# Kernel optimization log

Measured on AMD Instinct MI355X. Metric: run time of the kernel, lower is better.

Reference implementation:

```python
import jax, jax.numpy as jnp
import numpy as np
from jax.scipy.linalg import solve_triangular

H, VD, M = 16, 64, 128
RIDGE = 0.01


def setup_inputs() -> dict:
    key = jax.random.key(0)
    ks = jax.random.split(key, 9)
    B, L, HD = 4, 2048, 1024
    s = 1.0 / np.sqrt(HD).astype(np.float32)
    return {
        "x": jax.random.normal(ks[0], (B, L, HD), dtype=jnp.float32),
        "cur_k": jnp.zeros((1,), dtype=jnp.float32),
        "input_mask": jnp.ones((B, L), dtype=jnp.float32),
        "Wq": jax.random.normal(ks[1], (HD, HD), dtype=jnp.float32) * s,
        "Wk": jax.random.normal(ks[2], (HD, HD), dtype=jnp.float32) * s,
        "Wv": jax.random.normal(ks[3], (HD, HD), dtype=jnp.float32) * s,
        "Wo": jax.random.normal(ks[4], (HD, HD), dtype=jnp.float32) * s,
        "bo": jax.random.normal(ks[5], (HD,), dtype=jnp.float32) * s,
        "rff_W": jax.random.normal(ks[6], (H, VD, M), dtype=jnp.float32),  # / lengthscale=1.0
        "rff_b": 2.0 * np.pi * jax.random.uniform(ks[7], (H, M), dtype=jnp.float32),
    }


def reference(x, cur_k, input_mask, Wq, Wk, Wv, Wo, bo, rff_W, rff_b):
    B, L, HD = x.shape
    scale = jnp.asarray(1.0 / np.sqrt(M), dtype=x.dtype)
    M2 = 2 * M

    def heads(t):  # [B,L,HD] -> [B,H,L,VD]
        return t.reshape(B, L, H, VD).transpose(0, 2, 1, 3)

    q = heads(x @ Wq.T)
    k = heads(x @ Wk.T)
    v = heads(x @ Wv.T)

    mask = input_mask[:, :L].astype(x.dtype)
    qmask = mask[:, None, :, None]  # [B,1,L,1]

    def rff(X):  # [B,H,L,VD] -> [B,H,L,2M]
        proj = jnp.einsum('bhld,hdm->bhlm', X, rff_W) + rff_b[None, :, None, :]
        return scale * jnp.concatenate([jnp.cos(proj), jnp.sin(proj)], axis=-1)

    PhiQ = rff(q)
    PhiK_w = rff(k) * qmask
    V_w = v * qmask

    G = jnp.einsum('bhlm,bhln->bhmn', PhiK_w, PhiK_w)  # [B,H,2M,2M]
    G = G + RIDGE * jnp.eye(M2, dtype=x.dtype)
    T = jnp.einsum('bhlm,bhld->bhmd', PhiK_w, V_w)      # [B,H,2M,VD]

    Lch = jnp.linalg.cholesky(G)
    y = solve_triangular(Lch, T, lower=True)
    W = solve_triangular(jnp.swapaxes(Lch, -2, -1), y, lower=False)

    out = jnp.einsum('bhlm,bhmd->bhld', PhiQ, W)        # [B,H,L,VD]
    # unsqueeze sample dim, permute to [B,1,L,H,VD], flatten heads -> [B,1,L,HD]
    samples = jnp.transpose(out, (0, 2, 1, 3)).reshape(B, L, HD)[:, None]
    samples = samples @ Wo.T + bo                        # W_O (dropout: eval no-op)
    samples = samples * qmask                            # [B,1,L,1] broadcast
    return samples
```

## Files before the change

### kernel.cpp

```cpp
#include <hip/hip_runtime.h>
#include <math.h>

#define B_ 4
#define L_ 2048
#define HD_ 1024
#define H_ 16
#define VD_ 64
#define M_ 128
#define M2_ 256
#define RIDGE_ 0.01f
#define SCALE_ 0.08838834764831845f

typedef unsigned short u16;
typedef __attribute__((ext_vector_type(8))) short short8;
typedef __attribute__((ext_vector_type(4))) float floatx4;

__device__ __forceinline__ u16 f2bf(float x) {
  unsigned u = __float_as_uint(x);
  unsigned r = u + 0x7fff + ((u >> 16) & 1);
  return (u16)(r >> 16);
}
__device__ __forceinline__ float bf2f(u16 h) {
  return __uint_as_float(((unsigned)h) << 16);
}
__device__ __forceinline__ void gload_lds16(const u16* g, u16* l) {
  __builtin_amdgcn_global_load_lds(
      (const __attribute__((address_space(1))) unsigned int*)g,
      (__attribute__((address_space(3))) unsigned int*)l, 16, 0, 0);
}
__device__ __forceinline__ void split4(float4 f, ushort4* h, float4* r) {
  h->x = f2bf(f.x); h->y = f2bf(f.y); h->z = f2bf(f.z); h->w = f2bf(f.w);
  r->x = f.x - bf2f(h->x); r->y = f.y - bf2f(h->y);
  r->z = f.z - bf2f(h->z); r->w = f.w - bf2f(h->w);
}
#define WAITVM(N) asm volatile("s_waitcnt vmcnt(" #N ")" ::: "memory")
__device__ __forceinline__ void barf() {
  asm volatile("" ::: "memory");
  __builtin_amdgcn_s_barrier();
  asm volatile("" ::: "memory");
}
__device__ __forceinline__ void swz2d(int* bx, int* by) {
  int gx = gridDim.x;
  int nwg = gx * gridDim.y;
  int orig = (*by) * gx + (*bx);
  int wg = (orig & 7) * (nwg >> 3) + (orig >> 3);
  *bx = wg % gx;
  *by = wg / gx;
}

__global__ __launch_bounds__(256) void cvt_split_kernel(
    const float* __restrict__ src, u16* __restrict__ hi, u16* __restrict__ lo, int n4)
{
  int i = blockIdx.x * 256 + threadIdx.x;
  if (i < n4) {
    float4 f = ((const float4*)src)[i];
    ushort4 hv; float4 r;
    split4(f, &hv, &r);
    ushort4 lv = {f2bf(r.x), f2bf(r.y), f2bf(r.z), f2bf(r.w)};
    ((ushort4*)hi)[i] = hv;
    ((ushort4*)lo)[i] = lv;
  }
}

__global__ __launch_bounds__(256) void mfma_nt(
    const u16* __restrict__ A0, const u16* __restrict__ B0,
    float* __restrict__ C, int Ndim, int Kdim, int ldA, int ldB,
    const float* __restrict__ bias, const float* __restrict__ mask)
{
  __shared__ __align__(16) u16 a_sm[2][4096];
  __shared__ __align__(16) u16 b_sm[2][4096];
  const int tid = threadIdx.x;
  const int wave = tid >> 6, lane = tid & 63;
  int bx = blockIdx.x, by = blockIdx.y;
  swz2d(&bx, &by);
  const int m0 = by * 128, n0 = bx * 128;
  const int wrow = (wave >> 1) * 64, wcol = (wave & 1) * 64;
  const int fm = lane & 15, q = lane >> 4;
  const int lofs = wave * 1024;

  floatx4 acc[4][4];
#pragma unroll
  for (int i = 0; i < 4; ++i)
#pragma unroll
    for (int j = 0; j < 4; ++j) acc[i][j] = (floatx4){0.f, 0.f, 0.f, 0.f};

  const u16* Ag0 = A0 + (long)(m0 + lane) * ldA + wave * 8;
  const u16* Ag1 = A0 + (long)(m0 + 64 + lane) * ldA + wave * 8;
  const u16* Bg0 = B0 + (long)(n0 + lane) * ldB + wave * 8;
  const u16* Bg1 = B0 + (long)(n0 + 64 + lane) * ldB + wave * 8;

  auto stage = [&](int d, int k0) {
    gload_lds16(Ag0 + k0, &a_sm[d][lofs]);
    gload_lds16(Ag1 + k0, &a_sm[d][lofs + 512]);
    gload_lds16(Bg0 + k0, &b_sm[d][lofs]);
    gload_lds16(Bg1 + k0, &b_sm[d][lofs + 512]);
  };
  auto compute = [&](int d) {
    short8 af[4], bfv[4];
#pragma unroll
    for (int i = 0; i < 4; ++i)
      af[i] = *(const short8*)&a_sm[d][(q * 128 + wrow + i * 16 + fm) * 8];
#pragma unroll
    for (int j = 0; j < 4; ++j)
      bfv[j] = *(const short8*)&b_sm[d][(q * 128 + wcol + j * 16 + fm) * 8];
    __builtin_amdgcn_s_setprio(1);
#pragma unroll
    for (int i = 0; i < 4; ++i)
#pragma unroll
      for (int j = 0; j < 4; ++j)
        acc[i][j] = __builtin_amdgcn_mfma_f32_16x16x32_bf16(af[i], bfv[j], acc[i][j], 0, 0, 0);
    __builtin_amdgcn_s_setprio(0);
  };

  stage(0, 0);
  stage(1, 32);
  for (int k = 0; k + 64 < Kdim; k += 64) {
    WAITVM(4); barf();
    compute(0);
    barf();
    stage(0, k + 64);
    WAITVM(4); barf();
    compute(1);
    barf();
    stage(1, k + 96);
  }
  WAITVM(4); barf();
  compute(0);
  barf();
  WAITVM(0); barf();
  compute(1);

  const int colb = n0 + wcol + fm;
  const int rbase = m0 + wrow + (lane >> 4) * 4;
#pragma unroll
  for (int j = 0; j < 4; ++j) {
    int cg = colb + j * 16;
    float bb = bias ? bias[cg] : 0.f;
#pragma unroll
    for (int i = 0; i < 4; ++i) {
#pragma unroll
      for (int r = 0; r < 4; ++r) {
        int row = rbase + i * 16 + r;
        float val = acc[i][j][r];
        if (bias) val = (val + bb) * mask[row];
        C[(long)row * Ndim + cg] = val;
      }
    }
  }
}

__global__ __launch_bounds__(256) void mfma_qk3(
    const u16* __restrict__ Ah, const u16* __restrict__ Al,
    const u16* __restrict__ Bh, const u16* __restrict__ Bl,
    float* __restrict__ Cq, float* __restrict__ Ck)
{
  __shared__ __align__(16) u16 ah_sm[2][4096], al_sm[2][4096];
  __shared__ __align__(16) u16 bh_sm[2][4096], bl_sm[2][4096];
  const int tid = threadIdx.x;
  const int wave = tid >> 6, lane = tid & 63;
  int bx = blockIdx.x, by = blockIdx.y;
  swz2d(&bx, &by);
  const int m0 = by * 128, n0 = bx * 128;
  const int wrow = (wave >> 1) * 64, wcol = (wave & 1) * 64;
  const int fm = lane & 15, q = lane >> 4;
  const int lofs = wave * 1024;

  floatx4 acc[4][4];
#pragma unroll
  for (int i = 0; i < 4; ++i)
#pragma unroll
    for (int j = 0; j < 4; ++j) acc[i][j] = (floatx4){0.f, 0.f, 0.f, 0.f};

  const long a0o = (long)(m0 + lane) * 1024 + wave * 8;
  const long a1o = (long)(m0 + 64 + lane) * 1024 + wave * 8;
  const long b0o = (long)(n0 + lane) * 1024 + wave * 8;
  const long b1o = (long)(n0 + 64 + lane) * 1024 + wave * 8;

  auto stage = [&](int d, int k0) {
    gload_lds16(Ah + a0o + k0, &ah_sm[d][lofs]);
    gload_lds16(Ah + a1o + k0, &ah_sm[d][lofs + 512]);
    gload_lds16(Al + a0o + k0, &al_sm[d][lofs]);
    gload_lds16(Al + a1o + k0, &al_sm[d][lofs + 512]);
    gload_lds16(Bh + b0o + k0, &bh_sm[d][lofs]);
    gload_lds16(Bh + b1o + k0, &bh_sm[d][lofs + 512]);
    gload_lds16(Bl + b0o + k0, &bl_sm[d][lofs]);
    gload_lds16(Bl + b1o + k0, &bl_sm[d][lofs + 512]);
  };
  auto compute = [&](int d) {
    short8 afh[4], afl[4], bfh[4], bfl[4];
#pragma unroll
    for (int i = 0; i < 4; ++i) {
      afh[i] = *(const short8*)&ah_sm[d][(q * 128 + wrow + i * 16 + fm) * 8];
      afl[i] = *(const short8*)&al_sm[d][(q * 128 + wrow + i * 16 + fm) * 8];
    }
#pragma unroll
    for (int j = 0; j < 4; ++j) {
      bfh[j] = *(const short8*)&bh_sm[d][(q * 128 + wcol + j * 16 + fm) * 8];
      bfl[j] = *(const short8*)&bl_sm[d][(q * 128 + wcol + j * 16 + fm) * 8];
    }
    __builtin_amdgcn_s_setprio(1);
#pragma unroll
    for (int i = 0; i < 4; ++i)
#pragma unroll
      for (int j = 0; j < 4; ++j) {
        acc[i][j] = __builtin_amdgcn_mfma_f32_16x16x32_bf16(afh[i], bfh[j], acc[i][j], 0, 0, 0);
        acc[i][j] = __builtin_amdgcn_mfma_f32_16x16x32_bf16(afl[i], bfh[j], acc[i][j], 0, 0, 0);
        acc[i][j] = __builtin_amdgcn_mfma_f32_16x16x32_bf16(afh[i], bfl[j], acc[i][j], 0, 0, 0);
      }
    __builtin_amdgcn_s_setprio(0);
  };

  stage(0, 0);
  stage(1, 32);
  for (int k = 0; k + 64 < 1024; k += 64) {
    WAITVM(8); barf();
    compute(0);
    barf();
    stage(0, k + 64);
    WAITVM(8); barf();
    compute(1);
    barf();
    stage(1, k + 96);
  }
  WAITVM(8); barf();
  compute(0);
  barf();
  WAITVM(0); barf();
  compute(1);

  float* Cp; int cb;
  if (n0 < 1024) { Cp = Cq; cb = n0; }
  else           { Cp = Ck; cb = n0 - 1024; }
  const int colb = cb + wcol + fm;
  const int rbase = m0 + wrow + (lane >> 4) * 4;
#pragma unroll
  for (int j = 0; j < 4; ++j) {
    int cg = colb + j * 16;
#pragma unroll
    for (int i = 0; i < 4; ++i)
#pragma unroll
      for (int r = 0; r < 4; ++r)
        Cp[(long)(rbase + i * 16 + r) * 1024 + cg] = acc[i][j][r];
  }
}

__global__ __launch_bounds__(256) void rff_k_t(
    const float* __restrict__ src, const float* __restrict__ mask,
    const float* __restrict__ rffW, const float* __restrict__ rffb,
    u16* __restrict__ pkh, u16* __restrict__ pkl, int b0)
{
  __shared__ __align__(16) float w_lds[64][132];
  __shared__ __align__(16) float x_lds[64][68];
  __shared__ float b_lds[128];
  const int l0 = blockIdx.x * 64;
  const int h = blockIdx.y, b = b0 + blockIdx.z;
  const int zloc = blockIdx.z * 16 + h;
  const int tid = threadIdx.x;

  const float* wsrc = rffW + h * 8192;
  for (int f = tid * 4; f < 8192; f += 1024) {
    int d = f >> 7, m = f & 127;
    *(float4*)&w_lds[d][m] = *(const float4*)&wsrc[f];
  }
  if (tid < 128) b_lds[tid] = rffb[h * 128 + tid];
  {
    int r = tid >> 2, c0 = (tid & 3) * 16;
    const float* srow = src + (long)(b * L_ + l0 + r) * 1024 + h * VD_ + c0;
    *(float4*)&x_lds[r][c0 + 0]  = *(const float4*)(srow + 0);
    *(float4*)&x_lds[r][c0 + 4]  = *(const float4*)(srow + 4);
    *(float4*)&x_lds[r][c0 + 8]  = *(const float4*)(srow + 8);
    *(float4*)&x_lds[r][c0 + 12] = *(const float4*)(srow + 12);
  }
  __syncthreads();

  const int ty = tid >> 4, tx = tid & 15;
  float acc[4][8];
  {
    float4 bb0 = *(const float4*)&b_lds[4 * tx];
    float4 bb1 = *(const float4*)&b_lds[4 * tx + 64];
#pragma unroll
    for (int i = 0; i < 4; ++i) {
      acc[i][0] = bb0.x; acc[i][1] = bb0.y; acc[i][2] = bb0.z; acc[i][3] = bb0.w;
      acc[i][4] = bb1.x; acc[i][5] = bb1.y; acc[i][6] = bb1.z; acc[i][7] = bb1.w;
    }
  }
#pragma unroll 8
  for (int kk = 0; kk < 64; ++kk) {
    float4 w0 = *(const float4*)&w_lds[kk][4 * tx];
    float4 w1 = *(const float4*)&w_lds[kk][4 * tx + 64];
    float xv[4];
#pragma unroll
    for (int i = 0; i < 4; ++i) xv[i] = x_lds[4 * ty + i][kk];
#pragma unroll
    for (int i = 0; i < 4; ++i) {
      acc[i][0] = fmaf(xv[i], w0.x, acc[i][0]);
      acc[i][1] = fmaf(xv[i], w0.y, acc[i][1]);
      acc[i][2] = fmaf(xv[i], w0.z, acc[i][2]);
      acc[i][3] = fmaf(xv[i], w0.w, acc[i][3]);
      acc[i][4] = fmaf(xv[i], w1.x, acc[i][4]);
      acc[i][5] = fmaf(xv[i], w1.y, acc[i][5]);
      acc[i][6] = fmaf(xv[i], w1.z, acc[i][6]);
      acc[i][7] = fmaf(xv[i], w1.w, acc[i][7]);
    }
  }
  float fi[4];
#pragma unroll
  for (int i = 0; i < 4; ++i) fi[i] = SCALE_ * mask[b * L_ + l0 + 4 * ty + i];
  float cvv[4][8], svv[4][8];
#pragma unroll
  for (int i = 0; i < 4; ++i)
#pragma unroll
    for (int jj = 0; jj < 8; ++jj) {
      float sv, cv;
      sincosf(acc[i][jj], &sv, &cv);
      cvv[i][jj] = cv * fi[i];
      svv[i][jj] = sv * fi[i];
    }
  const long lbase = l0 + 4 * ty;
  const long zbase = (long)zloc * 655360;
#pragma unroll
  for (int jj = 0; jj < 8; ++jj) {
    int mcol = (jj < 4) ? (4 * tx + jj) : (64 + 4 * tx + (jj - 4));
    ushort4 h4, l4;
    h4.x = f2bf(cvv[0][jj]); l4.x = f2bf(cvv[0][jj] - bf2f(h4.x));
    h4.y = f2bf(cvv[1][jj]); l4.y = f2bf(cvv[1][jj] - bf2f(h4.y));
    h4.z = f2bf(cvv[2][jj]); l4.z = f2bf(cvv[2][jj] - bf2f(h4.z));
    h4.w = f2bf(cvv[3][jj]); l4.w = f2bf(cvv[3][jj] - bf2f(h4.w));
    long base = zbase + (long)mcol * 2048 + lbase;
    *(ushort4*)&pkh[base] = h4;
    *(ushort4*)&pkl[base] = l4;
    ushort4 hs, ls;
    hs.x = f2bf(svv[0][jj]); ls.x = f2bf(svv[0][jj] - bf2f(hs.x));
    hs.y = f2bf(svv[1][jj]); ls.y = f2bf(svv[1][jj] - bf2f(hs.y));
    hs.z = f2bf(svv[2][jj]); ls.z = f2bf(svv[2][jj] - bf2f(hs.z));
    hs.w = f2bf(svv[3][jj]); ls.w = f2bf(svv[3][jj] - bf2f(hs.w));
    long base2 = zbase + (long)(mcol + 128) * 2048 + lbase;
    *(ushort4*)&pkh[base2] = hs;
    *(ushort4*)&pkl[base2] = ls;
  }
}

__global__ __launch_bounds__(256) void vt_kernel(
    const float* __restrict__ v, const float* __restrict__ mask,
    u16* __restrict__ pkh, u16* __restrict__ pkl, int b0)
{
  __shared__ float t[128][65];
  const int z = blockIdx.y;
  const int b = b0 + (z >> 4), h = z & 15;
  const int l0 = blockIdx.x * 128;
  const int tid = threadIdx.x;
  const int d = tid & 63, lg = tid >> 6;
  for (int i = 0; i < 128; i += 4) {
    int ll = i + lg;
    float mv = mask[b * L_ + l0 + ll];
    t[ll][d] = v[(long)(b * L_ + l0 + ll) * 1024 + h * 64 + d] * mv;
  }
  __syncthreads();
  const int d2 = tid >> 2, lofs = (tid & 3) * 32;
  long base = (long)z * 655360 + (long)(256 + d2) * 2048 + l0 + lofs;
  for (int j = 0; j < 32; j += 4) {
    float f0 = t[lofs + j + 0][d2], f1 = t[lofs + j + 1][d2];
    float f2 = t[lofs + j + 2][d2], f3 = t[lofs + j + 3][d2];
    ushort4 hv, lv;
    hv.x = f2bf(f0); lv.x = f2bf(f0 - bf2f(hv.x));
    hv.y = f2bf(f1); lv.y = f2bf(f1 - bf2f(hv.y));
    hv.z = f2bf(f2); lv.z = f2bf(f2 - bf2f(hv.z));
    hv.w = f2bf(f3); lv.w = f2bf(f3 - bf2f(hv.w));
    *(ushort4*)&pkh[base + j] = hv;
    *(ushort4*)&pkl[base + j] = lv;
  }
}

__global__ __launch_bounds__(256) void mfma_gt(
    const u16* __restrict__ pkh, const u16* __restrict__ pkl,
    float* __restrict__ Gp, float* __restrict__ Tp, int bh0)
{
  __shared__ __align__(16) u16 ah_sm[2][4096], al_sm[2][4096];
  __shared__ __align__(16) u16 bh_sm[2][2048], bl_sm[2][2048];
  const int tid = threadIdx.x;
  const int wave = tid >> 6, lane = tid & 63;
  int orig = (blockIdx.z * gridDim.y + blockIdx.y) * gridDim.x + blockIdx.x;
  int wg = (orig & 7) * 64 + (orig >> 3);
  const int cx = wg & 7;
  const int rr = wg >> 3;
  const int kc = rr & 1;
  const int z = rr >> 1;
  int mt, n0;
  if (cx < 3) { mt = 0; n0 = (cx == 2) ? 256 : cx * 64; }
  else        { mt = 1; n0 = (cx - 3) * 64; }
  const int m0 = mt * 128;
  const int wrow = (wave >> 1) * 64, wcol = (wave & 1) * 32;
  const int fm = lane & 15, q = lane >> 4;
  const long batch = (long)z * 655360;
  const u16* Ahp = pkh + batch;
  const u16* Alp = pkl + batch;
  const int lofsA = wave * 1024;
  const int lofsB = wave * 512;

  floatx4 acc[4][2];
#pragma unroll
  for (int i = 0; i < 4; ++i)
#pragma unroll
    for (int j = 0; j < 2; ++j) acc[i][j] = (floatx4){0.f, 0.f, 0.f, 0.f};

  const long a0o = (long)(m0 + lane) * 2048 + wave * 8;
  const long a1o = (long)(m0 + 64 + lane) * 2048 + wave * 8;
  const long b0o = (long)(n0 + lane) * 2048 + wave * 8;

  auto stage = [&](int d, int k0) {
    gload_lds16(Ahp + a0o + k0, &ah_sm[d][lofsA]);
    gload_lds16(Ahp + a1o + k0, &ah_sm[d][lofsA + 512]);
    gload_lds16(Alp + a0o + k0, &al_sm[d][lofsA]);
    gload_lds16(Alp + a1o + k0, &al_sm[d][lofsA + 512]);
    gload_lds16(Ahp + b0o + k0, &bh_sm[d][lofsB]);
    gload_lds16(Alp + b0o + k0, &bl_sm[d][lofsB]);
  };
  auto compute = [&](int d) {
    short8 afh[4], afl[4], bfh[2], bfl[2];
#pragma unroll
    for (int i = 0; i < 4; ++i) {
      afh[i] = *(const short8*)&ah_sm[d][(q * 128 + wrow + i * 16 + fm) * 8];
      afl[i] = *(const short8*)&al_sm[d][(q * 128 + wrow + i * 16 + fm) * 8];
    }
#pragma unroll
    for (int j = 0; j < 2; ++j) {
      bfh[j] = *(const short8*)&bh_sm[d][(q * 64 + wcol + j * 16 + fm) * 8];
      bfl[j] = *(const short8*)&bl_sm[d][(q * 64 + wcol + j * 16 + fm) * 8];
    }
    __builtin_amdgcn_s_setprio(1);
#pragma unroll
    for (int i = 0; i < 4; ++i)
#pragma unroll
      for (int j = 0; j < 2; ++j) {
        acc[i][j] = __builtin_amdgcn_mfma_f32_16x16x32_bf16(afh[i], bfh[j], acc[i][j], 0, 0, 0);
        acc[i][j] = __builtin_amdgcn_mfma_f32_16x16x32_bf16(afl[i], bfh[j], acc[i][j], 0, 0, 0);
        acc[i][j] = __builtin_amdgcn_mfma_f32_16x16x32_bf16(afh[i], bfl[j], acc[i][j], 0, 0, 0);
      }
    __builtin_amdgcn_s_setprio(0);
  };

  const int kbeg = kc * 1024, kend = kbeg + 1024;
  stage(0, kbeg);
  stage(1, kbeg + 32);
  for (int k = kbeg; k + 64 < kend; k += 64) {
    WAITVM(6); barf();
    compute(0);
    barf();
    stage(0, k + 64);
    WAITVM(6); barf();
    compute(1);
    barf();
    stage(1, k + 96);
  }
  WAITVM(6); barf();
  compute(0);
  barf();
  WAITVM(0); barf();
  compute(1);

  const int bh = bh0 + z;
  float* Gb = Gp + (long)kc * 4194304;
  float* Tb = Tp + (long)kc * 1048576;
  const int rbase = m0 + wrow + (lane >> 4) * 4;
#pragma unroll
  for (int j = 0; j < 2; ++j) {
    int col = n0 + wcol + j * 16 + fm;
#pragma unroll
    for (int i = 0; i < 4; ++i)
#pragma unroll
      for (int r = 0; r < 4; ++r) {
        int row = rbase + i * 16 + r;
        float val = acc[i][j][r];
        if (n0 < 256) Gb[(long)bh * 65536 + (long)row * 256 + col] = val;
        else Tb[(long)bh * 16384 + (long)row * 64 + (col - 256)] = val;
      }
  }
}

__global__ __launch_bounds__(256) void reduce_gt_kernel(
    const float* __restrict__ Gp, float* __restrict__ G,
    const float* __restrict__ Tp, float* __restrict__ T)
{
  long i = (long)blockIdx.x * 256 + threadIdx.x;
  if (i < 1048576) {
    float4 a = ((const float4*)Gp)[i];
    float4 b = ((const float4*)(Gp + 4194304))[i];
    float4 o = {a.x + b.x, a.y + b.y, a.z + b.z, a.w + b.w};
    ((float4*)G)[i] = o;
  } else {
    long j = i - 1048576;
    float4 a = ((const float4*)Tp)[j];
    float4 b = ((const float4*)(Tp + 1048576))[j];
    float4 o = {a.x + b.x, a.y + b.y, a.z + b.z, a.w + b.w};
    ((float4*)T)[j] = o;
  }
}

__global__ __launch_bounds__(256) void mfma_out_k(
    const u16* __restrict__ ph, const u16* __restrict__ pl,
    const u16* __restrict__ wth, const u16* __restrict__ wtl,
    u16* __restrict__ oh)
{
  __shared__ __align__(16) u16 ah_sm[2][4096], al_sm[2][4096];
  __shared__ __align__(16) u16 bh_sm[2][2048], bl_sm[2][2048];
  const int tid = threadIdx.x;
  const int wave = tid >> 6, lane = tid & 63;
  int bx = blockIdx.x, by = blockIdx.y;
  swz2d(&bx, &by);
  const int bh = by;
  const int b = bh >> 4, h = bh & 15;
  const int l0 = bx * 128;
  const int wrow = (wave >> 1) * 64, wcol = (wave & 1) * 32;
  const int fm = lane & 15, q = lane >> 4;
  const u16* Ahp = ph + (long)bh * 524288 + (long)l0 * 256;
  const u16* Alp = pl + (long)bh * 524288 + (long)l0 * 256;
  const u16* Bhp = wth + (long)bh * 16384;
  const u16* Blp = wtl + (long)bh * 16384;
  const int lofsA = wave * 1024;
  const int lofsB = wave * 512;

  floatx4 acc[4][2];
#pragma unroll
  for (int i = 0; i < 4; ++i)
#pragma unroll
    for (int j = 0; j < 2; ++j) acc[i][j] = (floatx4){0.f, 0.f, 0.f, 0.f};

  const long a0o = (long)lane * 256 + wave * 8;
  const long a1o = (long)(64 + lane) * 256 + wave * 8;
  const long b0o = (long)lane * 256 + wave * 8;

  auto stage = [&](int d, int k0) {
    gload_lds16(Ahp + a0o + k0, &ah_sm[d][lofsA]);
    gload_lds16(Ahp + a1o + k0, &ah_sm[d][lofsA + 512]);
    gload_lds16(Alp + a0o + k0, &al_sm[d][lofsA]);
    gload_lds16(Alp + a1o + k0, &al_sm[d][lofsA + 512]);
    gload_lds16(Bhp + b0o + k0, &bh_sm[d][lofsB]);
    gload_lds16(Blp + b0o + k0, &bl_sm[d][lofsB]);
  };
  auto compute = [&](int d) {
    short8 afh[4], afl[4], bfh[2], bfl[2];
#pragma unroll
    for (int i = 0; i < 4; ++i) {
      afh[i] = *(const short8*)&ah_sm[d][(q * 128 + wrow + i * 16 + fm) * 8];
      afl[i] = *(const short8*)&al_sm[d][(q * 128 + wrow + i * 16 + fm) * 8];
    }
#pragma unroll
    for (int j = 0; j < 2; ++j) {
      bfh[j] = *(const short8*)&bh_sm[d][(q * 64 + wcol + j * 16 + fm) * 8];
      bfl[j] = *(const short8*)&bl_sm[d][(q * 64 + wcol + j * 16 + fm) * 8];
    }
    __builtin_amdgcn_s_setprio(1);
#pragma unroll
    for (int i = 0; i < 4; ++i)
#pragma unroll
      for (int j = 0; j < 2; ++j) {
        acc[i][j] = __builtin_amdgcn_mfma_f32_16x16x32_bf16(afh[i], bfh[j], acc[i][j], 0, 0, 0);
        acc[i][j] = __builtin_amdgcn_mfma_f32_16x16x32_bf16(afl[i], bfh[j], acc[i][j], 0, 0, 0);
        acc[i][j] = __builtin_amdgcn_mfma_f32_16x16x32_bf16(afh[i], bfl[j], acc[i][j], 0, 0, 0);
      }
    __builtin_amdgcn_s_setprio(0);
  };

  stage(0, 0);
  stage(1, 32);
  for (int k = 0; k + 64 < 256; k += 64) {
    WAITVM(6); barf();
    compute(0);
    barf();
    stage(0, k + 64);
    WAITVM(6); barf();
    compute(1);
    barf();
    stage(1, k + 96);
  }
  WAITVM(6); barf();
  compute(0);
  barf();
  WAITVM(0); barf();
  compute(1);

  const int rbase = l0 + wrow + (lane >> 4) * 4;
#pragma unroll
  for (int j = 0; j < 2; ++j) {
    int col = h * 64 + wcol + j * 16 + fm;
#pragma unroll
    for (int i = 0; i < 4; ++i)
#pragma unroll
      for (int r = 0; r < 4; ++r)
        oh[(long)(b * L_ + rbase + i * 16 + r) * 1024 + col] = f2bf(acc[i][j][r]);
  }
}

__global__ __launch_bounds__(512) void chol_rffq_wo_kernel(
    float* __restrict__ Gw,
    const float* __restrict__ qsrc,
    const float* __restrict__ rffW, const float* __restrict__ rffb,
    u16* __restrict__ ph, u16* __restrict__ pl,
    const float* __restrict__ Wo, u16* __restrict__ wo_hi)
{
  extern __shared__ float sm[];
  const int bx = blockIdx.x;
  const int tid = threadIdx.x;

  if (bx < 64) {
    float* panel = sm;
    float* invD  = sm + 4352;
    float* Gb = Gw + (long)bx * 65536;

    for (int p = 0; p < 16; ++p) {
      if (tid < 64) {
        const int i = tid & 15;
        float r[16];
#pragma unroll
        for (int k = 0; k < 16; ++k) r[k] = Gb[(16 * p + i) * 256 + 16 * p + k];
        r[i] += RIDGE_;
#pragma unroll
        for (int j = 0; j < 16; ++j) {
          float dj = __shfl(r[j], j);
          float dinv = 1.0f / sqrtf(dj);
          r[j] *= dinv;
          float Lij = r[j];
#pragma unroll
          for (int k = j + 1; k < 16; ++k) {
            float Lkj = __shfl(r[j], k);
            r[k] = fmaf(-Lij, Lkj, r[k]);
          }
        }
        float x[16];
#pragma unroll
        for (int j = 0; j < 16; ++j) {
          float s = (i == j) ? 1.0f : 0.0f;
#pragma unroll
          for (int k = 0; k < j; ++k) {
            float Ljk = __shfl(r[k], j);
            s = fmaf(-Ljk, x[k], s);
          }
          float Ljj = __shfl(r[j], j);
          x[j] = s / Ljj;
        }
        if (tid < 16) {
#pragma unroll
          for (int j = 0; j < 16; ++j) {
            invD[j * 17 + tid] = x[j];
            Gb[(16 * p + j) * 256 + 16 * p + tid] = x[j];
          }
        }
      }
      __syncthreads();

      const int nIb = 15 - p;
      if (nIb == 0) break;
      const int nrows = nIb * 16;
      const int r0 = 16 * (p + 1);

      for (int f = tid; f < nrows * 16; f += 512) {
        int rr = f >> 4, cc = f & 15;
        panel[(r0 + rr) * 17 + cc] = Gb[(long)(r0 + rr) * 256 + 16 * p + cc];
      }
      __syncthreads();

      float outv[8];
#pragma unroll
      for (int s = 0; s < 8; ++s) {
        int f = tid + s * 512;
        if (f < nrows * 16) {
          int rr = f >> 4, j = f & 15;
          const float* arow = &panel[(r0 + rr) * 17];
          const float* dcol = &invD[j * 17];
          float s2 = 0.f;
#pragma unroll
          for (int k = 0; k < 16; ++k) s2 = fmaf(arow[k], dcol[k], s2);
          outv[s] = s2;
        }
      }
      __syncthreads();
#pragma unroll
      for (int s = 0; s < 8; ++s) {
        int f = tid + s * 512;
        if (f < nrows * 16) {
          int rr = f >> 4, j = f & 15;
          panel[(r0 + rr) * 17 + j] = outv[s];
          Gb[(long)(r0 + rr) * 256 + 16 * p + j] = outv[s];
        }
      }
      __syncthreads();

      const int npairs = nIb * (nIb + 1) / 2;
      const int g = tid >> 4, t = tid & 15;
      const int tx = t & 3, ty = t >> 2;
      for (int pi0 = 0; pi0 < npairs; pi0 += 32) {
        int pi = pi0 + g;
        if (pi < npairs) {
          int a = 0; while ((a + 1) * (a + 2) / 2 <= pi) ++a;
          int b2 = pi - a * (a + 1) / 2;
          int I = p + 1 + a, J = p + 1 + b2;
          float c4[4][4];
#pragma unroll
          for (int ii = 0; ii < 4; ++ii) {
            float4 cv = *(const float4*)&Gb[(long)(16 * I + 4 * ty + ii) * 256 + 16 * J + 4 * tx];
            c4[ii][0] = cv.x; c4[ii][1] = cv.y; c4[ii][2] = cv.z; c4[ii][3] = cv.w;
          }
#pragma unroll
          for (int kk = 0; kk < 16; ++kk) {
            float av[4], bv[4];
#pragma unroll
            for (int ii = 0; ii < 4; ++ii) av[ii] = panel[(16 * I + 4 * ty + ii) * 17 + kk];
#pragma unroll
            for (int jj = 0; jj < 4; ++jj) bv[jj] = panel[(16 * J + 4 * tx + jj) * 17 + kk];
#pragma unroll
            for (int ii = 0; ii < 4; ++ii)
#pragma unroll
              for (int jj = 0; jj < 4; ++jj)
                c4[ii][jj] = fmaf(-av[ii], bv[jj], c4[ii][jj]);
          }
#pragma unroll
          for (int ii = 0; ii < 4; ++ii) {
            float4 cv = {c4[ii][0], c4[ii][1], c4[ii][2], c4[ii][3]};
            *(float4*)&Gb[(long)(16 * I + 4 * ty + ii) * 256 + 16 * J + 4 * tx] = cv;
          }
        }
      }
      __syncthreads();
    }
  } else if (bx < 64 + 2048) {
    const int id = bx - 64;
    const int l0 = (id & 31) * 64;
    const int h = (id >> 5) & 15;
    const int b = id >> 9;
    float* w_lds = sm;
    float* x_lds = sm + 8448;
    float* b_lds = sm + 12800;

    const float* wsrc = rffW + h * 8192;
    for (int f = tid * 4; f < 8192; f += 2048) {
      int d = f >> 7, m = f & 127;
      *(float4*)&w_lds[d * 132 + m] = *(const float4*)&wsrc[f];
    }
    if (tid < 128) b_lds[tid] = rffb[h * 128 + tid];
    {
      int r = tid >> 3, c0 = (tid & 7) * 8;
      const float* srow = qsrc + (long)(b * L_ + l0 + r) * 1024 + h * VD_ + c0;
      *(float4*)&x_lds[r * 68 + c0 + 0] = *(const float4*)(srow + 0);
      *(float4*)&x_lds[r * 68 + c0 + 4] = *(const float4*)(srow + 4);
    }
    __syncthreads();

    const int sub = tid >> 8;
    const int t = tid & 255;
    const int ty = t >> 4, tx = t & 15;
    const int rrow = sub * 32 + 2 * ty;
    float acc[2][8];
    {
      float4 bb0 = *(const float4*)&b_lds[4 * tx];
      float4 bb1 = *(const float4*)&b_lds[4 * tx + 64];
#pragma unroll
      for (int i = 0; i < 2; ++i) {
        acc[i][0] = bb0.x; acc[i][1] = bb0.y; acc[i][2] = bb0.z; acc[i][3] = bb0.w;
        acc[i][4] = bb1.x; acc[i][5] = bb1.y; acc[i][6] = bb1.z; acc[i][7] = bb1.w;
      }
    }
#pragma unroll 8
    for (int kk = 0; kk < 64; ++kk) {
      float4 w0 = *(const float4*)&w_lds[kk * 132 + 4 * tx];
      float4 w1 = *(const float4*)&w_lds[kk * 132 + 4 * tx + 64];
      float xv[2];
#pragma unroll
      for (int i = 0; i < 2; ++i) xv[i] = x_lds[(rrow + i) * 68 + kk];
#pragma unroll
      for (int i = 0; i < 2; ++i) {
        acc[i][0] = fmaf(xv[i], w0.x, acc[i][0]);
        acc[i][1] = fmaf(xv[i], w0.y, acc[i][1]);
        acc[i][2] = fmaf(xv[i], w0.z, acc[i][2]);
        acc[i][3] = fmaf(xv[i], w0.w, acc[i][3]);
        acc[i][4] = fmaf(xv[i], w1.x, acc[i][4]);
        acc[i][5] = fmaf(xv[i], w1.y, acc[i][5]);
        acc[i][6] = fmaf(xv[i], w1.z, acc[i][6]);
        acc[i][7] = fmaf(xv[i], w1.w, acc[i][7]);
      }
    }
#pragma unroll
    for (int i = 0; i < 2; ++i) {
      int l = l0 + rrow + i;
      float4 c0, c1, s0, s1;
      float sv, cv;
      sincosf(acc[i][0], &sv, &cv); c0.x = cv * SCALE_; s0.x = sv * SCALE_;
      sincosf(acc[i][1], &sv, &cv); c0.y = cv * SCALE_; s0.y = sv * SCALE_;
      sincosf(acc[i][2], &sv, &cv); c0.z = cv * SCALE_; s0.z = sv * SCALE_;
      sincosf(acc[i][3], &sv, &cv); c0.w = cv * SCALE_; s0.w = sv * SCALE_;
      sincosf(acc[i][4], &sv, &cv); c1.x = cv * SCALE_; s1.x = sv * SCALE_;
      sincosf(acc[i][5], &sv, &cv); c1.y = cv * SCALE_; s1.y = sv * SCALE_;
      sincosf(acc[i][6], &sv, &cv); c1.z = cv * SCALE_; s1.z = sv * SCALE_;
      sincosf(acc[i][7], &sv, &cv); c1.w = cv * SCALE_; s1.w = sv * SCALE_;
      long base = ((long)(b * H_ + h) * L_ + l) * M2_;
      ushort4 hv; float4 r4;
      split4(c0, &hv, &r4);
      *(ushort4*)&ph[base + 4 * tx] = hv;
      *(ushort4*)&pl[base + 4 * tx] = (ushort4){f2bf(r4.x), f2bf(r4.y), f2bf(r4.z), f2bf(r4.w)};
      split4(c1, &hv, &r4);
      *(ushort4*)&ph[base + 64 + 4 * tx] = hv;
      *(ushort4*)&pl[base + 64 + 4 * tx] = (ushort4){f2bf(r4.x), f2bf(r4.y), f2bf(r4.z), f2bf(r4.w)};
      split4(s0, &hv, &r4);
      *(ushort4*)&ph[base + 128 + 4 * tx] = hv;
      *(ushort4*)&pl[base + 128 + 4 * tx] = (ushort4){f2bf(r4.x), f2bf(r4.y), f2bf(r4.z), f2bf(r4.w)};
      split4(s1, &hv, &r4);
      *(ushort4*)&ph[base + 192 + 4 * tx] = hv;
      *(ushort4*)&pl[base + 192 + 4 * tx] = (ushort4){f2bf(r4.x), f2bf(r4.y), f2bf(r4.z), f2bf(r4.w)};
    }
  } else {
    const int id2 = bx - (64 + 2048);
    int idx = id2 * 512 + tid;
    for (int i = idx; i < 262144; i += 65536) {
      float4 f = ((const float4*)Wo)[i];
      ushort4 hv = {f2bf(f.x), f2bf(f.y), f2bf(f.z), f2bf(f.w)};
      ((ushort4*)wo_hi)[i] = hv;
    }
  }
}

__global__ __launch_bounds__(256) void tri_solve_kernel(
    const float* __restrict__ Gw, const float* __restrict__ T,
    u16* __restrict__ wth, u16* __restrict__ wtl)
{
  __shared__ float Y[256 * 17];
  __shared__ float tmp[16 * 17];
  const int bh = blockIdx.y;
  const int d0 = blockIdx.x * 16;
  const int tid = threadIdx.x;
  const int i = tid >> 4, d = tid & 15;
  const float* Gb = Gw + (long)bh * 65536;
  const float* Tb = T + (long)bh * 16384;

  for (int r = i; r < 256; r += 16) Y[r * 17 + d] = Tb[r * 64 + d0 + d];
  __syncthreads();

  for (int J = 0; J < 16; ++J) {
    float acc = Y[(J * 16 + i) * 17 + d];
    for (int c = 0; c < J; ++c) {
      const float* Lblk = &Gb[(long)(16 * J + i) * 256 + 16 * c];
#pragma unroll
      for (int k = 0; k < 16; k += 4) {
        float4 l4 = *(const float4*)&Lblk[k];
        acc = fmaf(-l4.x, Y[(c * 16 + k + 0) * 17 + d], acc);
        acc = fmaf(-l4.y, Y[(c * 16 + k + 1) * 17 + d], acc);
        acc = fmaf(-l4.z, Y[(c * 16 + k + 2) * 17 + d], acc);
        acc = fmaf(-l4.w, Y[(c * 16 + k + 3) * 17 + d], acc);
      }
    }
    tmp[i * 17 + d] = acc;
    __syncthreads();
    const float* invD = &Gb[(long)(16 * J + i) * 256 + 16 * J];
    float y = 0.f;
#pragma unroll
    for (int k = 0; k < 16; ++k) y = fmaf(invD[k], tmp[k * 17 + d], y);
    Y[(J * 16 + i) * 17 + d] = y;
    __syncthreads();
  }

  for (int J = 15; J >= 0; --J) {
    float acc = Y[(J * 16 + i) * 17 + d];
    for (int I = J + 1; I < 16; ++I) {
#pragma unroll
      for (int k = 0; k < 16; ++k)
        acc = fmaf(-Gb[(long)(16 * I + k) * 256 + 16 * J + i], Y[(I * 16 + k) * 17 + d], acc);
    }
    tmp[i * 17 + d] = acc;
    __syncthreads();
    float w = 0.f;
#pragma unroll
    for (int k = 0; k < 16; ++k)
      w = fmaf(Gb[(long)(16 * J + k) * 256 + 16 * J + i], tmp[k * 17 + d], w);
    Y[(J * 16 + i) * 17 + d] = w;
    __syncthreads();
  }

  for (int f = tid; f < 16 * 256; f += 256) {
    int dc = f >> 8, m = f & 255;
    float val = Y[m * 17 + dc];
    u16 h = f2bf(val);
    long o = (long)bh * 16384 + (long)(d0 + dc) * 256 + m;
    wth[o] = h;
    wtl[o] = f2bf(val - bf2f(h));
  }
}

__global__ void ws_too_small_kernel(float* out) { out[0] = 12345.0f; }

extern "C" void kernel_launch(void* const* d_in, const int* in_sizes, int n_in,
                              void* d_out, int out_size, void* d_ws, size_t ws_size,
                              hipStream_t stream) {
  const float* x    = (const float*)d_in[0];
  const float* mask = (const float*)d_in[2];
  const float* Wq   = (const float*)d_in[3];
  const float* Wk   = (const float*)d_in[4];
  const float* Wv   = (const float*)d_in[5];
  const float* Wo   = (const float*)d_in[6];
  const float* bo   = (const float*)d_in[7];
  const float* rffW = (const float*)d_in[8];
  const float* rffb = (const float*)d_in[9];
  float* out = (float*)d_out;
  float* ws  = (float*)d_ws;

  const size_t needed = 58720256UL * 4UL;
  if (ws_size < needed) {
    ws_too_small_kernel<<<1, 1, 0, stream>>>(out);
    return;
  }
  float* q = ws;
  u16* oh_bf = (u16*)ws;
  float* kbuf = ws + 8388608;
  float* T    = ws + 8388608;
  float* G    = ws + 9437184;
  u16* big16 = (u16*)(ws + 16777216);
  u16* x_hi = big16;
  u16* x_lo = big16 + 8388608;
  u16* w_hi = big16 + 16777216;
  u16* w_lo = big16 + 19922944;
  u16* pk_hi = big16;
  u16* pk_lo = big16 + 20971520;
  float* Gp = ws + 37748736;
  float* Tp = ws + 46137344;
  u16* phiq_hi = big16;
  u16* phiq_lo = big16 + 33554432;
  float* v = ws + 50331648;
  u16* wt_hi = (u16*)(ws + 50331648);
  u16* wt_lo = wt_hi + 1048576;
  u16* wo_hi = wt_hi + 2097152;

  hipFuncSetAttribute((const void*)chol_rffq_wo_kernel,
                      hipFuncAttributeMaxDynamicSharedMemorySize, 51712);

  dim3 blk(256);

  cvt_split_kernel<<<8192, blk, 0, stream>>>(x, x_hi, x_lo, 2097152);
  cvt_split_kernel<<<1024, blk, 0, stream>>>(Wq, w_hi,           w_lo,           262144);
  cvt_split_kernel<<<1024, blk, 0, stream>>>(Wk, w_hi + 1048576, w_lo + 1048576, 262144);
  cvt_split_kernel<<<1024, blk, 0, stream>>>(Wv, w_hi + 2097152, w_lo + 2097152, 262144);

  mfma_qk3<<<dim3(16, 64), blk, 0, stream>>>(x_hi, x_lo, w_hi, w_lo, q, kbuf);
  mfma_nt<<<dim3(8, 64), blk, 0, stream>>>(x_hi, w_hi + 2097152, v,
                                           1024, 1024, 1024, 1024, nullptr, nullptr);

  for (int half = 0; half < 2; ++half) {
    int b0 = half * 2, bh0 = half * 32;
    rff_k_t<<<dim3(32, 16, 2), blk, 0, stream>>>(kbuf, mask, rffW, rffb, pk_hi, pk_lo, b0);
    vt_kernel<<<dim3(16, 32), blk, 0, stream>>>(v, mask, pk_hi, pk_lo, b0);
    mfma_gt<<<dim3(8, 2, 32), blk, 0, stream>>>(pk_hi, pk_lo, Gp, Tp, bh0);
  }

  reduce_gt_kernel<<<5120, blk, 0, stream>>>(Gp, G, Tp, T);

  chol_rffq_wo_kernel<<<dim3(64 + 2048 + 128), dim3(512), 51712, stream>>>(
      G, q, rffW, rffb, phiq_hi, phiq_lo, Wo, wo_hi);

  tri_solve_kernel<<<dim3(4, 64), dim3(256), 0, stream>>>(G, T, wt_hi, wt_lo);

  mfma_out_k<<<dim3(16, 64), blk, 0, stream>>>(phiq_hi, phiq_lo, wt_hi, wt_lo, oh_bf);

  mfma_nt<<<dim3(8, 64), blk, 0, stream>>>(oh_bf, wo_hi, out, 1024, 1024, 1024, 1024, bo, mask);
}
```

Baseline: 814.5 us.

## Keep Cholesky next panel in LDS and software-pipeline trailing updates

The blocked Cholesky now holds the next 16-column panel in shared memory: it is loaded once at the start, and the trailing update writes the next panel's tiles to LDS instead of global memory. This removes the per-step global panel reload and one barrier. The trailing-update loop is double-buffered, prefetching the next tile's global C block while the current one computes, and the LDS reads are vectorised as float4 with a stride of 20. It raises register and LDS use, and the Cholesky blocks are a small share of the total work.

```diff
diff --git a/kernel.cpp b/kernel.cpp
--- a/kernel.cpp
+++ b/kernel.cpp
@@ -595,7 +595,7 @@
     float* __restrict__ Gw,
     const float* __restrict__ qsrc,
     const float* __restrict__ rffW, const float* __restrict__ rffb,
-    u16* __restrict__ ph, u16* __restrict__ pl,
+    u16* __restrict__ ph, u16* __restrict__ pl_out,
     const float* __restrict__ Wo, u16* __restrict__ wo_hi)
 {
   extern __shared__ float sm[];
@@ -603,16 +603,23 @@
   const int tid = threadIdx.x;
 
   if (bx < 64) {
-    float* panel = sm;
-    float* invD  = sm + 4352;
+    float* pa   = sm;
+    float* plds = sm + 5120;
+    float* invD = sm + 10240;
     float* Gb = Gw + (long)bx * 65536;
+
+    for (int f = tid; f < 4096; f += 512) {
+      int rr = f >> 4, cc = f & 15;
+      pa[rr * 20 + cc] = Gb[rr * 256 + cc];
+    }
+    __syncthreads();
 
     for (int p = 0; p < 16; ++p) {
       if (tid < 64) {
         const int i = tid & 15;
         float r[16];
 #pragma unroll
-        for (int k = 0; k < 16; ++k) r[k] = Gb[(16 * p + i) * 256 + 16 * p + k];
+        for (int k = 0; k < 16; ++k) r[k] = pa[(16 * p + i) * 20 + k];
         r[i] += RIDGE_;
 #pragma unroll
         for (int j = 0; j < 16; ++j) {
@@ -641,7 +648,7 @@
         if (tid < 16) {
 #pragma unroll
           for (int j = 0; j < 16; ++j) {
-            invD[j * 17 + tid] = x[j];
+            invD[j * 20 + tid] = x[j];
             Gb[(16 * p + j) * 256 + 16 * p + tid] = x[j];
           }
         }
@@ -653,34 +660,25 @@
       const int nrows = nIb * 16;
       const int r0 = 16 * (p + 1);
 
-      for (int f = tid; f < nrows * 16; f += 512) {
-        int rr = f >> 4, cc = f & 15;
-        panel[(r0 + rr) * 17 + cc] = Gb[(long)(r0 + rr) * 256 + 16 * p + cc];
-      }
-      __syncthreads();
-
-      float outv[8];
 #pragma unroll
       for (int s = 0; s < 8; ++s) {
         int f = tid + s * 512;
         if (f < nrows * 16) {
           int rr = f >> 4, j = f & 15;
-          const float* arow = &panel[(r0 + rr) * 17];
-          const float* dcol = &invD[j * 17];
+          const float* arow = &pa[(r0 + rr) * 20];
+          const float* dcol = &invD[j * 20];
           float s2 = 0.f;
 #pragma unroll
-          for (int k = 0; k < 16; ++k) s2 = fmaf(arow[k], dcol[k], s2);
-          outv[s] = s2;
-        }
-      }
-      __syncthreads();
-#pragma unroll
-      for (int s = 0; s < 8; ++s) {
-        int f = tid + s * 512;
-        if (f < nrows * 16) {
-          int rr = f >> 4, j = f & 15;
-          panel[(r0 + rr) * 17 + j] = outv[s];
-          Gb[(long)(r0 + rr) * 256 + 16 * p + j] = outv[s];
+          for (int k4 = 0; k4 < 16; k4 += 4) {
+            float4 a4 = *(const float4*)&arow[k4];
+            float4 d4 = *(const float4*)&dcol[k4];
+            s2 = fmaf(a4.x, d4.x, s2);
+            s2 = fmaf(a4.y, d4.y, s2);
+            s2 = fmaf(a4.z, d4.z, s2);
+            s2 = fmaf(a4.w, d4.w, s2);
+          }
+          plds[(r0 + rr) * 20 + j] = s2;
+          Gb[(long)(r0 + rr) * 256 + 16 * p + j] = s2;
         }
       }
       __syncthreads();
@@ -688,37 +686,74 @@
       const int npairs = nIb * (nIb + 1) / 2;
       const int g = tid >> 4, t = tid & 15;
       const int tx = t & 3, ty = t >> 2;
+
+      int IA = 0, JA = 0;
+      float c4a[4][4];
+      bool va = g < npairs;
+      if (va) {
+        int a = 0; while ((a + 1) * (a + 2) / 2 <= g) ++a;
+        int b2 = g - a * (a + 1) / 2;
+        IA = p + 1 + a; JA = p + 1 + b2;
+#pragma unroll
+        for (int ii = 0; ii < 4; ++ii) {
+          float4 cv = *(const float4*)&Gb[(long)(16 * IA + 4 * ty + ii) * 256 + 16 * JA + 4 * tx];
+          c4a[ii][0] = cv.x; c4a[ii][1] = cv.y; c4a[ii][2] = cv.z; c4a[ii][3] = cv.w;
+        }
+      }
       for (int pi0 = 0; pi0 < npairs; pi0 += 32) {
-        int pi = pi0 + g;
-        if (pi < npairs) {
-          int a = 0; while ((a + 1) * (a + 2) / 2 <= pi) ++a;
-          int b2 = pi - a * (a + 1) / 2;
-          int I = p + 1 + a, J = p + 1 + b2;
-          float c4[4][4];
+        int IB = 0, JB = 0;
+        float c4b[4][4];
+        int piB = pi0 + 32 + g;
+        bool vb = piB < npairs;
+        if (vb) {
+          int a = 0; while ((a + 1) * (a + 2) / 2 <= piB) ++a;
+          int b2 = piB - a * (a + 1) / 2;
+          IB = p + 1 + a; JB = p + 1 + b2;
 #pragma unroll
           for (int ii = 0; ii < 4; ++ii) {
-            float4 cv = *(const float4*)&Gb[(long)(16 * I + 4 * ty + ii) * 256 + 16 * J + 4 * tx];
-            c4[ii][0] = cv.x; c4[ii][1] = cv.y; c4[ii][2] = cv.z; c4[ii][3] = cv.w;
-          }
-#pragma unroll
-          for (int kk = 0; kk < 16; ++kk) {
-            float av[4], bv[4];
-#pragma unroll
-            for (int ii = 0; ii < 4; ++ii) av[ii] = panel[(16 * I + 4 * ty + ii) * 17 + kk];
-#pragma unroll
-            for (int jj = 0; jj < 4; ++jj) bv[jj] = panel[(16 * J + 4 * tx + jj) * 17 + kk];
-#pragma unroll
-            for (int ii = 0; ii < 4; ++ii)
-#pragma unroll
-              for (int jj = 0; jj < 4; ++jj)
-                c4[ii][jj] = fmaf(-av[ii], bv[jj], c4[ii][jj]);
-          }
-#pragma unroll
-          for (int ii = 0; ii < 4; ++ii) {
-            float4 cv = {c4[ii][0], c4[ii][1], c4[ii][2], c4[ii][3]};
-            *(float4*)&Gb[(long)(16 * I + 4 * ty + ii) * 256 + 16 * J + 4 * tx] = cv;
+            float4 cv = *(const float4*)&Gb[(long)(16 * IB + 4 * ty + ii) * 256 + 16 * JB + 4 * tx];
+            c4b[ii][0] = cv.x; c4b[ii][1] = cv.y; c4b[ii][2] = cv.z; c4b[ii][3] = cv.w;
           }
         }
+        if (va) {
+#pragma unroll
+          for (int k4 = 0; k4 < 16; k4 += 4) {
+            float4 a4[4], b4[4];
+#pragma unroll
+            for (int ii = 0; ii < 4; ++ii)
+              a4[ii] = *(const float4*)&plds[(16 * IA + 4 * ty + ii) * 20 + k4];
+#pragma unroll
+            for (int jj = 0; jj < 4; ++jj)
+              b4[jj] = *(const float4*)&plds[(16 * JA + 4 * tx + jj) * 20 + k4];
+#pragma unroll
+            for (int ii = 0; ii < 4; ++ii)
+#pragma unroll
+              for (int jj = 0; jj < 4; ++jj) {
+                c4a[ii][jj] = fmaf(-a4[ii].x, b4[jj].x, c4a[ii][jj]);
+                c4a[ii][jj] = fmaf(-a4[ii].y, b4[jj].y, c4a[ii][jj]);
+                c4a[ii][jj] = fmaf(-a4[ii].z, b4[jj].z, c4a[ii][jj]);
+                c4a[ii][jj] = fmaf(-a4[ii].w, b4[jj].w, c4a[ii][jj]);
+              }
+          }
+          if (JA == p + 1) {
+#pragma unroll
+            for (int ii = 0; ii < 4; ++ii) {
+              float4 cv = {c4a[ii][0], c4a[ii][1], c4a[ii][2], c4a[ii][3]};
+              *(float4*)&pa[(16 * IA + 4 * ty + ii) * 20 + 4 * tx] = cv;
+            }
+          } else {
+#pragma unroll
+            for (int ii = 0; ii < 4; ++ii) {
+              float4 cv = {c4a[ii][0], c4a[ii][1], c4a[ii][2], c4a[ii][3]};
+              *(float4*)&Gb[(long)(16 * IA + 4 * ty + ii) * 256 + 16 * JA + 4 * tx] = cv;
+            }
+          }
+        }
+        va = vb; IA = IB; JA = JB;
+#pragma unroll
+        for (int ii = 0; ii < 4; ++ii)
+#pragma unroll
+          for (int jj = 0; jj < 4; ++jj) c4a[ii][jj] = c4b[ii][jj];
       }
       __syncthreads();
     }
@@ -795,16 +830,16 @@
       ushort4 hv; float4 r4;
       split4(c0, &hv, &r4);
       *(ushort4*)&ph[base + 4 * tx] = hv;
-      *(ushort4*)&pl[base + 4 * tx] = (ushort4){f2bf(r4.x), f2bf(r4.y), f2bf(r4.z), f2bf(r4.w)};
+      *(ushort4*)&pl_out[base + 4 * tx] = (ushort4){f2bf(r4.x), f2bf(r4.y), f2bf(r4.z), f2bf(r4.w)};
       split4(c1, &hv, &r4);
       *(ushort4*)&ph[base + 64 + 4 * tx] = hv;
-      *(ushort4*)&pl[base + 64 + 4 * tx] = (ushort4){f2bf(r4.x), f2bf(r4.y), f2bf(r4.z), f2bf(r4.w)};
+      *(ushort4*)&pl_out[base + 64 + 4 * tx] = (ushort4){f2bf(r4.x), f2bf(r4.y), f2bf(r4.z), f2bf(r4.w)};
       split4(s0, &hv, &r4);
       *(ushort4*)&ph[base + 128 + 4 * tx] = hv;
-      *(ushort4*)&pl[base + 128 + 4 * tx] = (ushort4){f2bf(r4.x), f2bf(r4.y), f2bf(r4.z), f2bf(r4.w)};
+      *(ushort4*)&pl_out[base + 128 + 4 * tx] = (ushort4){f2bf(r4.x), f2bf(r4.y), f2bf(r4.z), f2bf(r4.w)};
       split4(s1, &hv, &r4);
       *(ushort4*)&ph[base + 192 + 4 * tx] = hv;
-      *(ushort4*)&pl[base + 192 + 4 * tx] = (ushort4){f2bf(r4.x), f2bf(r4.y), f2bf(r4.z), f2bf(r4.w)};
+      *(ushort4*)&pl_out[base + 192 + 4 * tx] = (ushort4){f2bf(r4.x), f2bf(r4.y), f2bf(r4.z), f2bf(r4.w)};
     }
   } else {
     const int id2 = bx - (64 + 2048);
```

Result: faster. 779.1 us (median of 2 runs) (-4.3%).
